# Performance work log

Hardware: AMD Instinct MI355X
Metric: run time of the kernel (lower is better)

The kernel has to match this reference:

```python
import jax, jax.numpy as jnp
import numpy as np

N_NODES = 100000
N_EDGES = 1600000
IN_C, HID, N_CLS = 128, 128, 40


def setup_inputs() -> dict:
    key = jax.random.key(0)
    ks = jax.random.split(key, 8)
    x = jax.random.normal(ks[0], (N_NODES, IN_C), dtype=jnp.float32)
    edge_index = jax.random.randint(ks[1], (2, N_EDGES), 0, N_NODES, dtype=jnp.int64)
    s1 = 1.0 / np.sqrt(IN_C)
    s2 = 1.0 / np.sqrt(HID)
    return {
        "x": x,
        "edge_index": edge_index,
        "Wl1": jax.random.normal(ks[2], (IN_C, HID), dtype=jnp.float32) * s1,
        "Wr1": jax.random.normal(ks[3], (IN_C, HID), dtype=jnp.float32) * s1,
        "b1": jnp.zeros((HID,), dtype=jnp.float32),
        "Wl2": jax.random.normal(ks[4], (HID, N_CLS), dtype=jnp.float32) * s2,
        "Wr2": jax.random.normal(ks[5], (HID, N_CLS), dtype=jnp.float32) * s2,
        "b2": jnp.zeros((N_CLS,), dtype=jnp.float32),
    }


def _sage_conv(x, src, dst, Wl, Wr, b):
    # mean-aggregate neighbor features at destination nodes
    n = x.shape[0]
    agg = jax.ops.segment_sum(x[src], dst, num_segments=n)           # [N, C]
    cnt = jax.ops.segment_sum(jnp.ones((src.shape[0],), x.dtype), dst, num_segments=n)
    mean = agg / jnp.maximum(cnt, 1.0)[:, None]
    return mean @ Wl + x @ Wr + b


def reference(x, edge_index, Wl1, Wr1, b1, Wl2, Wr2, b2):
    src, dst = edge_index[0], edge_index[1]
    h = jax.nn.relu(_sage_conv(x, src, dst, Wl1, Wr1, b1))
    return _sage_conv(h, src, dst, Wl2, Wr2, b2)
```

## Files before the change

### kernel.cpp

```cpp
#include <hip/hip_runtime.h>

#define C_IN 128
#define N_CLS 40
#define ZSTR 40

#define NPB   256
#define MAXNB 512
#define CAP   6144

typedef __attribute__((ext_vector_type(8))) short bf16x8;
typedef __attribute__((ext_vector_type(4))) float f32x4;
typedef __attribute__((ext_vector_type(2))) float f32x2;

__device__ __forceinline__ ushort f2b(float f) {
  union { float f; unsigned u; } v; v.f = f;
  unsigned r = v.u + 0x7FFF + ((v.u >> 16) & 1);
  return (ushort)(r >> 16);
}
__device__ __forceinline__ unsigned packbf(float lo, float hi) {
  return (unsigned)f2b(lo) | ((unsigned)f2b(hi) << 16);
}
__device__ __forceinline__ void acc2(float& fa, float& fb, unsigned u) {
  union { unsigned u; float f; } lo, hi;
  lo.u = u << 16; hi.u = u & 0xFFFF0000u;
  fa += lo.f; fb += hi.f;
}

#if __has_builtin(__builtin_amdgcn_cvt_pk_f32_fp8) && __has_builtin(__builtin_amdgcn_cvt_pk_fp8_f32)
#define HW_FP8 1
#else
#define HW_FP8 0
#endif

__device__ __forceinline__ float f8dec1(unsigned b) {
  unsigned E = (b >> 3) & 15, M = b & 7;
  if (E) {
    union { unsigned u; float f; } v;
    v.u = ((b & 0x80u) << 24) | ((E + 120u) << 23) | (M << 20);
    return v.f;
  }
  float m = (float)(int)M * 0.001953125f;
  return (b & 0x80u) ? -m : m;
}
__device__ __forceinline__ unsigned f8enc1(float x) {
  union { float f; unsigned u; } v; v.f = x;
  unsigned s = (v.u >> 31) << 7;
  float ax = fabsf(x);
  if (ax < 9.765625e-4f) return s;
  if (ax < 0.015625f) {
    int M = (int)rintf(ax * 512.0f);
    return (M >= 8) ? (s | 0x08u) : (s | (unsigned)M);
  }
  if (ax > 448.0f) return s | 0x7Eu;
  unsigned au = v.u & 0x7FFFFFFFu;
  unsigned r = au + 0x7FFFFu + ((au >> 20) & 1);
  int e = (int)(r >> 23) - 127;
  unsigned M = (r >> 20) & 7;
  if (e > 8) return s | 0x7Eu;
  return s | ((unsigned)(e + 7) << 3) | M;
}
__device__ __forceinline__ void accf8x4(float* a, unsigned u) {
#if HW_FP8
  f32x2 lo = __builtin_amdgcn_cvt_pk_f32_fp8((int)u, false);
  f32x2 hi = __builtin_amdgcn_cvt_pk_f32_fp8((int)u, true);
  a[0] += lo[0]; a[1] += lo[1]; a[2] += hi[0]; a[3] += hi[1];
#else
  a[0] += f8dec1(u & 0xFF); a[1] += f8dec1((u >> 8) & 0xFF);
  a[2] += f8dec1((u >> 16) & 0xFF); a[3] += f8dec1(u >> 24);
#endif
}
__device__ __forceinline__ unsigned packf8x4(float x0, float x1, float x2, float x3) {
#if HW_FP8
  int p = 0;
  p = __builtin_amdgcn_cvt_pk_fp8_f32(x0, x1, p, false);
  p = __builtin_amdgcn_cvt_pk_fp8_f32(x2, x3, p, true);
  return (unsigned)p;
#else
  return f8enc1(x0) | (f8enc1(x1) << 8) | (f8enc1(x2) << 16) | (f8enc1(x3) << 24);
#endif
}

__global__ __launch_bounds__(256) void bin_cvt_kernel(
    const int* __restrict__ src, const int* __restrict__ dst,
    int* __restrict__ bcur, unsigned* __restrict__ staged, int E, int NB, int nbin,
    const float* __restrict__ xin, ushort* __restrict__ xb,
    unsigned char* __restrict__ xf8, long n8)
{
  __shared__ int cnt[MAXNB];
  __shared__ int base[MAXNB];
  const int tid = threadIdx.x;
  if (blockIdx.x >= nbin) {
    long i = ((long)(blockIdx.x - nbin) * 256 + tid);
    if (i < n8) {
      const float4 a = *reinterpret_cast<const float4*>(xin + i * 8);
      const float4 b = *reinterpret_cast<const float4*>(xin + i * 8 + 4);
      uint4 o;
      o.x = packbf(a.x, a.y);
      o.y = packbf(a.z, a.w);
      o.z = packbf(b.x, b.y);
      o.w = packbf(b.z, b.w);
      *reinterpret_cast<uint4*>(xb + i * 8) = o;
      uint2 p;
      p.x = packf8x4(a.x, a.y, a.z, a.w);
      p.y = packf8x4(b.x, b.y, b.z, b.w);
      *reinterpret_cast<uint2*>(xf8 + i * 8) = p;
    }
    return;
  }
  for (int i = tid; i < NB; i += 256) cnt[i] = 0;
  __syncthreads();
  const int e0 = blockIdx.x * 4096;
  const int eend = min(e0 + 4096, E);
  for (int e = e0 + tid; e < eend; e += 256)
    atomicAdd(&cnt[dst[e] >> 8], 1);
  __syncthreads();
  for (int i = tid; i < NB; i += 256) {
    int c = cnt[i];
    base[i] = (c > 0) ? atomicAdd(&bcur[i], c) : 0;
    cnt[i] = 0;
  }
  __syncthreads();
  for (int e = e0 + tid; e < eend; e += 256) {
    int d = dst[e];
    int b = d >> 8;
    int pos = base[b] + atomicAdd(&cnt[b], 1);
    if (pos < CAP)
      staged[(size_t)b * CAP + pos] = (unsigned)src[e] | ((unsigned)(d & 255) << 20);
  }
}

__global__ __launch_bounds__(256) void csr_kernel(
    const unsigned* __restrict__ staged, const int* __restrict__ bcur,
    int* __restrict__ row_ptr, int* __restrict__ deg, int* __restrict__ csr_src, int N)
{
  __shared__ unsigned st[CAP];
  __shared__ int dcnt[NPB];
  __shared__ int cur[NPB];
  __shared__ int wsum[4];
  __shared__ int rb_s;
  const int b = blockIdx.x, tid = threadIdx.x;
  const int cb = min(bcur[b], CAP);
  for (int i = tid; i < cb; i += 256) st[i] = staged[(size_t)b * CAP + i];
  int part = 0;
  for (int i = tid; i < b; i += 256) part += min(bcur[i], CAP);
  if (tid == 0) rb_s = 0;
  dcnt[tid] = 0;
  __syncthreads();
  #pragma unroll
  for (int off = 32; off > 0; off >>= 1) part += __shfl_down(part, off);
  if ((tid & 63) == 0 && part != 0) atomicAdd(&rb_s, part);
  for (int i = tid; i < cb; i += 256) atomicAdd(&dcnt[st[i] >> 20], 1);
  __syncthreads();
  const int rb = rb_s;
  int d = dcnt[tid];
  const int lane = tid & 63, w = tid >> 6;
  int inc = d;
  #pragma unroll
  for (int off = 1; off < 64; off <<= 1) {
    int v = __shfl_up(inc, off);
    if (lane >= off) inc += v;
  }
  if (lane == 63) wsum[w] = inc;
  __syncthreads();
  int wo = 0;
  for (int i = 0; i < w; ++i) wo += wsum[i];
  const int excl = wo + inc - d;
  cur[tid] = excl;
  const int node = b * NPB + tid;
  if (node < N) { row_ptr[node] = rb + excl; deg[node] = d; }
  __syncthreads();
  for (int i = tid; i < cb; i += 256) {
    unsigned wv = st[i];
    int p = atomicAdd(&cur[wv >> 20], 1);
    csr_src[rb + p] = (int)(wv & 0xFFFFF);
  }
}

__global__ __launch_bounds__(256) void agg1_kernel(
    const unsigned char* __restrict__ xf8, const ushort* __restrict__ xb,
    const int* __restrict__ csr_src, const int* __restrict__ row_ptr,
    const int* __restrict__ deg, ushort* __restrict__ mean, int N)
{
  int t = blockIdx.x * 256 + threadIdx.x;
  int n = t >> 3;
  if (n >= N) return;
  int q = t & 7;
  int base = row_ptr[n];
  int d = deg[n];
  float a[16];
  #pragma unroll
  for (int i = 0; i < 16; ++i) a[i] = 0.f;
  if (d > 8) {
    const unsigned char* fq = xf8 + q * 16;
    int j = 0;
    for (; j + 4 <= d; j += 4) {
      int s0 = csr_src[base + j + 0];
      int s1 = csr_src[base + j + 1];
      int s2 = csr_src[base + j + 2];
      int s3 = csr_src[base + j + 3];
      uint4 v0 = *reinterpret_cast<const uint4*>(fq + (size_t)s0 * C_IN);
      uint4 v1 = *reinterpret_cast<const uint4*>(fq + (size_t)s1 * C_IN);
      uint4 v2 = *reinterpret_cast<const uint4*>(fq + (size_t)s2 * C_IN);
      uint4 v3 = *reinterpret_cast<const uint4*>(fq + (size_t)s3 * C_IN);
      accf8x4(a+0, v0.x); accf8x4(a+4, v0.y); accf8x4(a+8, v0.z); accf8x4(a+12, v0.w);
      accf8x4(a+0, v1.x); accf8x4(a+4, v1.y); accf8x4(a+8, v1.z); accf8x4(a+12, v1.w);
      accf8x4(a+0, v2.x); accf8x4(a+4, v2.y); accf8x4(a+8, v2.z); accf8x4(a+12, v2.w);
      accf8x4(a+0, v3.x); accf8x4(a+4, v3.y); accf8x4(a+8, v3.z); accf8x4(a+12, v3.w);
    }
    for (; j < d; ++j) {
      int s = csr_src[base + j];
      uint4 v = *reinterpret_cast<const uint4*>(fq + (size_t)s * C_IN);
      accf8x4(a+0, v.x); accf8x4(a+4, v.y); accf8x4(a+8, v.z); accf8x4(a+12, v.w);
    }
  } else {
    const ushort* fq = xb + q * 16;
    for (int j = 0; j < d; ++j) {
      int s = csr_src[base + j];
      uint4 w0 = *reinterpret_cast<const uint4*>(fq + (size_t)s * C_IN);
      uint4 w1 = *reinterpret_cast<const uint4*>(fq + (size_t)s * C_IN + 8);
      acc2(a[0],a[1],w0.x); acc2(a[2],a[3],w0.y); acc2(a[4],a[5],w0.z); acc2(a[6],a[7],w0.w);
      acc2(a[8],a[9],w1.x); acc2(a[10],a[11],w1.y); acc2(a[12],a[13],w1.z); acc2(a[14],a[15],w1.w);
    }
  }
  float inv = (d > 0) ? (1.0f / (float)d) : 0.0f;
  uint4 o0, o1;
  o0.x = packbf(a[0]*inv, a[1]*inv);  o0.y = packbf(a[2]*inv, a[3]*inv);
  o0.z = packbf(a[4]*inv, a[5]*inv);  o0.w = packbf(a[6]*inv, a[7]*inv);
  o1.x = packbf(a[8]*inv, a[9]*inv);  o1.y = packbf(a[10]*inv, a[11]*inv);
  o1.z = packbf(a[12]*inv, a[13]*inv); o1.w = packbf(a[14]*inv, a[15]*inv);
  uint4* mp = reinterpret_cast<uint4*>(mean + (size_t)n * C_IN + q * 16);
  mp[0] = o0;
  mp[1] = o1;
}

__global__ __launch_bounds__(256) void layer1_mfma(
    const ushort* __restrict__ xb, const ushort* __restrict__ mb,
    const float* __restrict__ Wr, const float* __restrict__ Wl,
    const float* __restrict__ bias, ushort* __restrict__ h, int N, int ntiles)
{
  __shared__ ushort sB[8 * 8 * 64 * 8];
  const int tid = threadIdx.x;
  for (int idx = tid; idx < 8 * 8 * 64; idx += 256) {
    int l  = idx & 63;
    int cg = (idx >> 6) & 7;
    int ks = idx >> 9;
    int c  = cg * 16 + (l & 15);
    int kb = ks * 32 + 8 * (l >> 4);
    ushort* p = &sB[idx * 8];
    #pragma unroll
    for (int j = 0; j < 8; ++j) {
      int k = kb + j;
      float w = (k < C_IN) ? Wr[k * C_IN + c] : Wl[(k - C_IN) * C_IN + c];
      p[j] = f2b(w);
    }
  }
  __syncthreads();
  const int w = tid >> 6, l = tid & 63;
  const int rfrag = l & 15, kg = l >> 4;
  for (int tile = blockIdx.x; tile < ntiles; tile += gridDim.x) {
    int n0 = tile * 128 + w * 32;
    int rc0 = n0 + rfrag;      rc0 = (rc0 < N) ? rc0 : (N - 1);
    int rc1 = n0 + 16 + rfrag; rc1 = (rc1 < N) ? rc1 : (N - 1);
    f32x4 acc[2][8] = {};
    #pragma unroll
    for (int ks = 0; ks < 8; ++ks) {
      int kb = ks * 32 + kg * 8;
      const ushort* Asrc = (kb < C_IN) ? (xb + kb) : (mb + (kb - C_IN));
      bf16x8 a0 = *reinterpret_cast<const bf16x8*>(Asrc + (size_t)rc0 * C_IN);
      bf16x8 a1 = *reinterpret_cast<const bf16x8*>(Asrc + (size_t)rc1 * C_IN);
      #pragma unroll
      for (int cg = 0; cg < 8; ++cg) {
        bf16x8 b = *reinterpret_cast<const bf16x8*>(&sB[((ks * 8 + cg) * 64 + l) * 8]);
        acc[0][cg] = __builtin_amdgcn_mfma_f32_16x16x32_bf16(a0, b, acc[0][cg], 0, 0, 0);
        acc[1][cg] = __builtin_amdgcn_mfma_f32_16x16x32_bf16(a1, b, acc[1][cg], 0, 0, 0);
      }
    }
    const int rowoff = (l >> 4) * 4, colbase = l & 15;
    #pragma unroll
    for (int f = 0; f < 2; ++f) {
      #pragma unroll
      for (int cg = 0; cg < 8; ++cg) {
        int c = cg * 16 + colbase;
        float bc = bias[c];
        #pragma unroll
        for (int r = 0; r < 4; ++r) {
          int row = n0 + f * 16 + rowoff + r;
          if (row < N) {
            float v = fmaxf(acc[f][cg][r] + bc, 0.0f);
            h[(size_t)row * C_IN + c] = f2b(v);
          }
        }
      }
    }
  }
}

__global__ __launch_bounds__(256) void gemm2_dual(
    const ushort* __restrict__ hb,
    const float* __restrict__ Wl, const float* __restrict__ Wr,
    ushort* __restrict__ z, float* __restrict__ out, int N, int ntiles)
{
  __shared__ ushort sBl[4 * 3 * 64 * 8];
  __shared__ ushort sBr[4 * 3 * 64 * 8];
  const int tid = threadIdx.x;
  for (int idx = tid; idx < 4 * 3 * 64; idx += 256) {
    int l  = idx & 63;
    int cg = (idx >> 6) % 3;
    int ks = idx / (3 * 64);
    int c  = cg * 16 + (l & 15);
    int kb = ks * 32 + 8 * (l >> 4);
    ushort* pl = &sBl[idx * 8];
    ushort* pr = &sBr[idx * 8];
    #pragma unroll
    for (int j = 0; j < 8; ++j) {
      int k = kb + j;
      float wl = 0.0f, wr = 0.0f;
      if (c < N_CLS) { wl = Wl[k * N_CLS + c]; wr = Wr[k * N_CLS + c]; }
      pl[j] = f2b(wl);
      pr[j] = f2b(wr);
    }
  }
  __syncthreads();
  const int w = tid >> 6, l = tid & 63;
  const int rfrag = l & 15, kg = l >> 4;
  for (int tile = blockIdx.x; tile < ntiles; tile += gridDim.x) {
    int n0 = tile * 128 + w * 32;
    int rc0 = n0 + rfrag;      rc0 = (rc0 < N) ? rc0 : (N - 1);
    int rc1 = n0 + 16 + rfrag; rc1 = (rc1 < N) ? rc1 : (N - 1);
    f32x4 az[2][3] = {};
    f32x4 ay[2][3] = {};
    #pragma unroll
    for (int ks = 0; ks < 4; ++ks) {
      int kb = ks * 32 + kg * 8;
      bf16x8 a0 = *reinterpret_cast<const bf16x8*>(hb + (size_t)rc0 * C_IN + kb);
      bf16x8 a1 = *reinterpret_cast<const bf16x8*>(hb + (size_t)rc1 * C_IN + kb);
      #pragma unroll
      for (int cg = 0; cg < 3; ++cg) {
        bf16x8 bl = *reinterpret_cast<const bf16x8*>(&sBl[((ks * 3 + cg) * 64 + l) * 8]);
        bf16x8 br = *reinterpret_cast<const bf16x8*>(&sBr[((ks * 3 + cg) * 64 + l) * 8]);
        az[0][cg] = __builtin_amdgcn_mfma_f32_16x16x32_bf16(a0, bl, az[0][cg], 0, 0, 0);
        az[1][cg] = __builtin_amdgcn_mfma_f32_16x16x32_bf16(a1, bl, az[1][cg], 0, 0, 0);
        ay[0][cg] = __builtin_amdgcn_mfma_f32_16x16x32_bf16(a0, br, ay[0][cg], 0, 0, 0);
        ay[1][cg] = __builtin_amdgcn_mfma_f32_16x16x32_bf16(a1, br, ay[1][cg], 0, 0, 0);
      }
    }
    const int rowoff = (l >> 4) * 4, colbase = l & 15;
    #pragma unroll
    for (int f = 0; f < 2; ++f) {
      #pragma unroll
      for (int cg = 0; cg < 3; ++cg) {
        int c = cg * 16 + colbase;
        if (c < N_CLS) {
          #pragma unroll
          for (int r = 0; r < 4; ++r) {
            int row = n0 + f * 16 + rowoff + r;
            if (row < N) {
              z[(size_t)row * ZSTR + c] = f2b(az[f][cg][r]);
              out[(size_t)row * N_CLS + c] = ay[f][cg][r];
            }
          }
        }
      }
    }
  }
}

__global__ __launch_bounds__(256) void agg2z_kernel(
    const ushort* __restrict__ z, const int* __restrict__ csr_src,
    const int* __restrict__ row_ptr, const int* __restrict__ deg,
    const float* __restrict__ b2, float* __restrict__ out, int N)
{
  unsigned w = blockIdx.x * 256 + threadIdx.x;
  unsigned n = w / 5u;
  if (n >= (unsigned)N) return;
  unsigned q = w - n * 5u;
  const ushort* zq = z + q * 8;
  int base = row_ptr[n];
  int d = deg[n];
  float a0=0.f,a1=0.f,a2=0.f,a3=0.f,a4=0.f,a5=0.f,a6=0.f,a7=0.f;
  int j = 0;
  for (; j + 4 <= d; j += 4) {
    int s0 = csr_src[base + j + 0];
    int s1 = csr_src[base + j + 1];
    int s2 = csr_src[base + j + 2];
    int s3 = csr_src[base + j + 3];
    uint4 v0 = *reinterpret_cast<const uint4*>(zq + (size_t)s0 * ZSTR);
    uint4 v1 = *reinterpret_cast<const uint4*>(zq + (size_t)s1 * ZSTR);
    uint4 v2 = *reinterpret_cast<const uint4*>(zq + (size_t)s2 * ZSTR);
    uint4 v3 = *reinterpret_cast<const uint4*>(zq + (size_t)s3 * ZSTR);
    acc2(a0,a1,v0.x); acc2(a2,a3,v0.y); acc2(a4,a5,v0.z); acc2(a6,a7,v0.w);
    acc2(a0,a1,v1.x); acc2(a2,a3,v1.y); acc2(a4,a5,v1.z); acc2(a6,a7,v1.w);
    acc2(a0,a1,v2.x); acc2(a2,a3,v2.y); acc2(a4,a5,v2.z); acc2(a6,a7,v2.w);
    acc2(a0,a1,v3.x); acc2(a2,a3,v3.y); acc2(a4,a5,v3.z); acc2(a6,a7,v3.w);
  }
  for (; j < d; ++j) {
    int s = csr_src[base + j];
    uint4 v = *reinterpret_cast<const uint4*>(zq + (size_t)s * ZSTR);
    acc2(a0,a1,v.x); acc2(a2,a3,v.y); acc2(a4,a5,v.z); acc2(a6,a7,v.w);
  }
  float inv = (d > 0) ? (1.0f / (float)d) : 0.0f;
  float* op = out + (size_t)n * N_CLS + q * 8;
  const float4 bA = *reinterpret_cast<const float4*>(b2 + q * 8);
  const float4 bB = *reinterpret_cast<const float4*>(b2 + q * 8 + 4);
  float4 y0 = *reinterpret_cast<const float4*>(op);
  float4 y1 = *reinterpret_cast<const float4*>(op + 4);
  y0.x += a0 * inv + bA.x; y0.y += a1 * inv + bA.y;
  y0.z += a2 * inv + bA.z; y0.w += a3 * inv + bA.w;
  y1.x += a4 * inv + bB.x; y1.y += a5 * inv + bB.y;
  y1.z += a6 * inv + bB.z; y1.w += a7 * inv + bB.w;
  *reinterpret_cast<float4*>(op) = y0;
  *reinterpret_cast<float4*>(op + 4) = y1;
}

extern "C" void kernel_launch(void* const* d_in, const int* in_sizes, int n_in,
                              void* d_out, int out_size, void* d_ws, size_t ws_size,
                              hipStream_t stream)
{
  const float* x   = (const float*)d_in[0];
  const int*   ei  = (const int*)d_in[1];
  const float* Wl1 = (const float*)d_in[2];
  const float* Wr1 = (const float*)d_in[3];
  const float* b1  = (const float*)d_in[4];
  const float* Wl2 = (const float*)d_in[5];
  const float* Wr2 = (const float*)d_in[6];
  const float* b2  = (const float*)d_in[7];
  float* out = (float*)d_out;

  const int N = in_sizes[0] / C_IN;
  const int E = in_sizes[1] / 2;
  const int* src = ei;
  const int* dst = ei + E;
  const int NB = (N + NPB - 1) / NPB;

  size_t Np = ((size_t)N + 255) & ~(size_t)255;
  size_t Ep = ((size_t)E + 255) & ~(size_t)255;
  int* wsi     = (int*)d_ws;
  int* bcur    = wsi;
  int* row_ptr = wsi + MAXNB;
  int* deg     = row_ptr + Np;
  int* csr_src = deg + Np;
  unsigned* staged = (unsigned*)(csr_src + Ep);
  ushort* zb    = (ushort*)staged;
  ushort* xb    = (ushort*)(staged + (size_t)MAXNB * CAP);
  ushort* meanb = xb + (size_t)N * C_IN;
  ushort* hb    = meanb + (size_t)N * C_IN;
  unsigned char* xf8 = (unsigned char*)(hb + (size_t)N * C_IN);

  hipMemsetAsync(bcur, 0, MAXNB * sizeof(int), stream);

  const int nbin = (E + 4095) / 4096;
  long n8 = (long)N * C_IN / 8;
  const int ncvt = (int)((n8 + 255) / 256);
  bin_cvt_kernel<<<nbin + ncvt, 256, 0, stream>>>(src, dst, bcur, staged, E, NB, nbin,
                                                  x, xb, xf8, n8);
  csr_kernel<<<NB, 256, 0, stream>>>(staged, bcur, row_ptr, deg, csr_src, N);

  const int ntiles = (N + 127) / 128;

  agg1_kernel<<<(N * 8 + 255) / 256, 256, 0, stream>>>(xf8, xb, csr_src, row_ptr, deg, meanb, N);
  layer1_mfma<<<512, 256, 0, stream>>>(xb, meanb, Wr1, Wl1, b1, hb, N, ntiles);

  gemm2_dual<<<512, 256, 0, stream>>>(hb, Wl2, Wr2, zb, out, N, ntiles);
  agg2z_kernel<<<(N * 5 + 255) / 256, 256, 0, stream>>>(zb, csr_src, row_ptr, deg, b2, out, N);
}
```

Baseline: 188.0 us.

## Store layer-2 Z in fp8, per-wave binning, pad bucket counters, move cvt to CSR

Layer-2 projected features z are now stored as fp8 instead of bf16, which halves the bytes gathered per neighbor in the second aggregation. The edge binning kernel uses per-wave shared counters and smaller edge chunks to cut LDS atomic contention. Global bucket counters are padded to separate cache lines. The x conversion work moves from the binning launch into the CSR launch, so conversion overlaps CSR building. The fp8 quantisation of z lowers output precision and adds accuracy risk.

```diff
diff --git a/kernel.cpp b/kernel.cpp
--- a/kernel.cpp
+++ b/kernel.cpp
@@ -2,11 +2,12 @@
 
 #define C_IN 128
 #define N_CLS 40
-#define ZSTR 40
+#define ZB   40
 
 #define NPB   256
 #define MAXNB 512
 #define CAP   6144
+#define BCSTR 16
 
 typedef __attribute__((ext_vector_type(8))) short bf16x8;
 typedef __attribute__((ext_vector_type(4))) float f32x4;
@@ -79,18 +80,66 @@
   return f8enc1(x0) | (f8enc1(x1) << 8) | (f8enc1(x2) << 16) | (f8enc1(x3) << 24);
 #endif
 }
-
-__global__ __launch_bounds__(256) void bin_cvt_kernel(
+__device__ __forceinline__ unsigned char f8enc_byte(float x) {
+#if HW_FP8
+  return (unsigned char)(__builtin_amdgcn_cvt_pk_fp8_f32(x, x, 0, false) & 0xFF);
+#else
+  return (unsigned char)f8enc1(x);
+#endif
+}
+
+__global__ __launch_bounds__(256) void bin_kernel(
     const int* __restrict__ src, const int* __restrict__ dst,
-    int* __restrict__ bcur, unsigned* __restrict__ staged, int E, int NB, int nbin,
+    int* __restrict__ bcur, unsigned* __restrict__ staged, int E, int NB)
+{
+  __shared__ int wcnt[4][MAXNB];
+  __shared__ int wbase[4][MAXNB];
+  const int tid = threadIdx.x;
+  const int wv = tid >> 6;
+  for (int i = tid; i < NB; i += 256) {
+    wcnt[0][i] = 0; wcnt[1][i] = 0; wcnt[2][i] = 0; wcnt[3][i] = 0;
+  }
+  __syncthreads();
+  const int e0 = blockIdx.x * 2048;
+  const int eend = min(e0 + 2048, E);
+  for (int e = e0 + tid; e < eend; e += 256)
+    atomicAdd(&wcnt[wv][dst[e] >> 8], 1);
+  __syncthreads();
+  for (int i = tid; i < NB; i += 256) {
+    int c0 = wcnt[0][i], c1 = wcnt[1][i], c2 = wcnt[2][i], c3 = wcnt[3][i];
+    int tot = c0 + c1 + c2 + c3;
+    int g = (tot > 0) ? atomicAdd(&bcur[i * BCSTR], tot) : 0;
+    wbase[0][i] = g;
+    wbase[1][i] = g + c0;
+    wbase[2][i] = g + c0 + c1;
+    wbase[3][i] = g + c0 + c1 + c2;
+    wcnt[0][i] = 0; wcnt[1][i] = 0; wcnt[2][i] = 0; wcnt[3][i] = 0;
+  }
+  __syncthreads();
+  for (int e = e0 + tid; e < eend; e += 256) {
+    int d = dst[e];
+    int b = d >> 8;
+    int pos = wbase[wv][b] + atomicAdd(&wcnt[wv][b], 1);
+    if (pos < CAP)
+      staged[(size_t)b * CAP + pos] = (unsigned)src[e] | ((unsigned)(d & 255) << 20);
+  }
+}
+
+__global__ __launch_bounds__(256) void csr_cvt_kernel(
+    const unsigned* __restrict__ staged, const int* __restrict__ bcur,
+    int* __restrict__ row_ptr, int* __restrict__ deg, int* __restrict__ csr_src,
+    int N, int NB,
     const float* __restrict__ xin, ushort* __restrict__ xb,
     unsigned char* __restrict__ xf8, long n8)
 {
-  __shared__ int cnt[MAXNB];
-  __shared__ int base[MAXNB];
+  __shared__ unsigned st[CAP];
+  __shared__ int dcnt[NPB];
+  __shared__ int cur[NPB];
+  __shared__ int wsum[4];
+  __shared__ int rb_s;
   const int tid = threadIdx.x;
-  if (blockIdx.x >= nbin) {
-    long i = ((long)(blockIdx.x - nbin) * 256 + tid);
+  if (blockIdx.x >= NB) {
+    long i = ((long)(blockIdx.x - NB) * 256 + tid);
     if (i < n8) {
       const float4 a = *reinterpret_cast<const float4*>(xin + i * 8);
       const float4 b = *reinterpret_cast<const float4*>(xin + i * 8 + 4);
@@ -107,42 +156,11 @@
     }
     return;
   }
-  for (int i = tid; i < NB; i += 256) cnt[i] = 0;
-  __syncthreads();
-  const int e0 = blockIdx.x * 4096;
-  const int eend = min(e0 + 4096, E);
-  for (int e = e0 + tid; e < eend; e += 256)
-    atomicAdd(&cnt[dst[e] >> 8], 1);
-  __syncthreads();
-  for (int i = tid; i < NB; i += 256) {
-    int c = cnt[i];
-    base[i] = (c > 0) ? atomicAdd(&bcur[i], c) : 0;
-    cnt[i] = 0;
-  }
-  __syncthreads();
-  for (int e = e0 + tid; e < eend; e += 256) {
-    int d = dst[e];
-    int b = d >> 8;
-    int pos = base[b] + atomicAdd(&cnt[b], 1);
-    if (pos < CAP)
-      staged[(size_t)b * CAP + pos] = (unsigned)src[e] | ((unsigned)(d & 255) << 20);
-  }
-}
-
-__global__ __launch_bounds__(256) void csr_kernel(
-    const unsigned* __restrict__ staged, const int* __restrict__ bcur,
-    int* __restrict__ row_ptr, int* __restrict__ deg, int* __restrict__ csr_src, int N)
-{
-  __shared__ unsigned st[CAP];
-  __shared__ int dcnt[NPB];
-  __shared__ int cur[NPB];
-  __shared__ int wsum[4];
-  __shared__ int rb_s;
-  const int b = blockIdx.x, tid = threadIdx.x;
-  const int cb = min(bcur[b], CAP);
+  const int b = blockIdx.x;
+  const int cb = min(bcur[b * BCSTR], CAP);
   for (int i = tid; i < cb; i += 256) st[i] = staged[(size_t)b * CAP + i];
   int part = 0;
-  for (int i = tid; i < b; i += 256) part += min(bcur[i], CAP);
+  for (int i = tid; i < b; i += 256) part += min(bcur[i * BCSTR], CAP);
   if (tid == 0) rb_s = 0;
   dcnt[tid] = 0;
   __syncthreads();
@@ -298,7 +316,7 @@
 __global__ __launch_bounds__(256) void gemm2_dual(
     const ushort* __restrict__ hb,
     const float* __restrict__ Wl, const float* __restrict__ Wr,
-    ushort* __restrict__ z, float* __restrict__ out, int N, int ntiles)
+    unsigned char* __restrict__ z, float* __restrict__ out, int N, int ntiles)
 {
   __shared__ ushort sBl[4 * 3 * 64 * 8];
   __shared__ ushort sBr[4 * 3 * 64 * 8];
@@ -355,7 +373,7 @@
           for (int r = 0; r < 4; ++r) {
             int row = n0 + f * 16 + rowoff + r;
             if (row < N) {
-              z[(size_t)row * ZSTR + c] = f2b(az[f][cg][r]);
+              z[(size_t)row * ZB + c] = f8enc_byte(az[f][cg][r]);
               out[(size_t)row * N_CLS + c] = ay[f][cg][r];
             }
           }
@@ -366,7 +384,7 @@
 }
 
 __global__ __launch_bounds__(256) void agg2z_kernel(
-    const ushort* __restrict__ z, const int* __restrict__ csr_src,
+    const unsigned char* __restrict__ z, const int* __restrict__ csr_src,
     const int* __restrict__ row_ptr, const int* __restrict__ deg,
     const float* __restrict__ b2, float* __restrict__ out, int N)
 {
@@ -374,29 +392,31 @@
   unsigned n = w / 5u;
   if (n >= (unsigned)N) return;
   unsigned q = w - n * 5u;
-  const ushort* zq = z + q * 8;
+  const unsigned char* zq = z + q * 8;
   int base = row_ptr[n];
   int d = deg[n];
-  float a0=0.f,a1=0.f,a2=0.f,a3=0.f,a4=0.f,a5=0.f,a6=0.f,a7=0.f;
+  float a[8];
+  #pragma unroll
+  for (int i = 0; i < 8; ++i) a[i] = 0.f;
   int j = 0;
   for (; j + 4 <= d; j += 4) {
     int s0 = csr_src[base + j + 0];
     int s1 = csr_src[base + j + 1];
     int s2 = csr_src[base + j + 2];
     int s3 = csr_src[base + j + 3];
-    uint4 v0 = *reinterpret_cast<const uint4*>(zq + (size_t)s0 * ZSTR);
-    uint4 v1 = *reinterpret_cast<const uint4*>(zq + (size_t)s1 * ZSTR);
-    uint4 v2 = *reinterpret_cast<const uint4*>(zq + (size_t)s2 * ZSTR);
-    uint4 v3 = *reinterpret_cast<const uint4*>(zq + (size_t)s3 * ZSTR);
-    acc2(a0,a1,v0.x); acc2(a2,a3,v0.y); acc2(a4,a5,v0.z); acc2(a6,a7,v0.w);
-    acc2(a0,a1,v1.x); acc2(a2,a3,v1.y); acc2(a4,a5,v1.z); acc2(a6,a7,v1.w);
-    acc2(a0,a1,v2.x); acc2(a2,a3,v2.y); acc2(a4,a5,v2.z); acc2(a6,a7,v2.w);
-    acc2(a0,a1,v3.x); acc2(a2,a3,v3.y); acc2(a4,a5,v3.z); acc2(a6,a7,v3.w);
+    uint2 v0 = *reinterpret_cast<const uint2*>(zq + (size_t)s0 * ZB);
+    uint2 v1 = *reinterpret_cast<const uint2*>(zq + (size_t)s1 * ZB);
+    uint2 v2 = *reinterpret_cast<const uint2*>(zq + (size_t)s2 * ZB);
+    uint2 v3 = *reinterpret_cast<const uint2*>(zq + (size_t)s3 * ZB);
+    accf8x4(a+0, v0.x); accf8x4(a+4, v0.y);
+    accf8x4(a+0, v1.x); accf8x4(a+4, v1.y);
+    accf8x4(a+0, v2.x); accf8x4(a+4, v2.y);
+    accf8x4(a+0, v3.x); accf8x4(a+4, v3.y);
   }
   for (; j < d; ++j) {
     int s = csr_src[base + j];
-    uint4 v = *reinterpret_cast<const uint4*>(zq + (size_t)s * ZSTR);
-    acc2(a0,a1,v.x); acc2(a2,a3,v.y); acc2(a4,a5,v.z); acc2(a6,a7,v.w);
+    uint2 v = *reinterpret_cast<const uint2*>(zq + (size_t)s * ZB);
+    accf8x4(a+0, v.x); accf8x4(a+4, v.y);
   }
   float inv = (d > 0) ? (1.0f / (float)d) : 0.0f;
   float* op = out + (size_t)n * N_CLS + q * 8;
@@ -404,10 +424,10 @@
   const float4 bB = *reinterpret_cast<const float4*>(b2 + q * 8 + 4);
   float4 y0 = *reinterpret_cast<const float4*>(op);
   float4 y1 = *reinterpret_cast<const float4*>(op + 4);
-  y0.x += a0 * inv + bA.x; y0.y += a1 * inv + bA.y;
-  y0.z += a2 * inv + bA.z; y0.w += a3 * inv + bA.w;
-  y1.x += a4 * inv + bB.x; y1.y += a5 * inv + bB.y;
-  y1.z += a6 * inv + bB.z; y1.w += a7 * inv + bB.w;
+  y0.x += a[0] * inv + bA.x; y0.y += a[1] * inv + bA.y;
+  y0.z += a[2] * inv + bA.z; y0.w += a[3] * inv + bA.w;
+  y1.x += a[4] * inv + bB.x; y1.y += a[5] * inv + bB.y;
+  y1.z += a[6] * inv + bB.z; y1.w += a[7] * inv + bB.w;
   *reinterpret_cast<float4*>(op) = y0;
   *reinterpret_cast<float4*>(op + 4) = y1;
 }
@@ -436,24 +456,25 @@
   size_t Ep = ((size_t)E + 255) & ~(size_t)255;
   int* wsi     = (int*)d_ws;
   int* bcur    = wsi;
-  int* row_ptr = wsi + MAXNB;
+  int* row_ptr = wsi + (size_t)MAXNB * BCSTR;
   int* deg     = row_ptr + Np;
   int* csr_src = deg + Np;
   unsigned* staged = (unsigned*)(csr_src + Ep);
-  ushort* zb    = (ushort*)staged;
+  unsigned char* zb = (unsigned char*)staged;
   ushort* xb    = (ushort*)(staged + (size_t)MAXNB * CAP);
   ushort* meanb = xb + (size_t)N * C_IN;
   ushort* hb    = meanb + (size_t)N * C_IN;
   unsigned char* xf8 = (unsigned char*)(hb + (size_t)N * C_IN);
 
-  hipMemsetAsync(bcur, 0, MAXNB * sizeof(int), stream);
-
-  const int nbin = (E + 4095) / 4096;
+  hipMemsetAsync(bcur, 0, (size_t)MAXNB * BCSTR * sizeof(int), stream);
+
+  const int nbin = (E + 2047) / 2048;
+  bin_kernel<<<nbin, 256, 0, stream>>>(src, dst, bcur, staged, E, NB);
+
   long n8 = (long)N * C_IN / 8;
   const int ncvt = (int)((n8 + 255) / 256);
-  bin_cvt_kernel<<<nbin + ncvt, 256, 0, stream>>>(src, dst, bcur, staged, E, NB, nbin,
-                                                  x, xb, xf8, n8);
-  csr_kernel<<<NB, 256, 0, stream>>>(staged, bcur, row_ptr, deg, csr_src, N);
+  csr_cvt_kernel<<<NB + ncvt, 256, 0, stream>>>(staged, bcur, row_ptr, deg, csr_src,
+                                                N, NB, x, xb, xf8, n8);
 
   const int ntiles = (N + 127) / 128;
 
```

Result: no change. 188.5 us (+0.3%).
